# Kernel tuning notes

Measured on AMD Instinct MI355X. Metric: run time of the kernel, lower is better.

Reference implementation:

```python
import jax, jax.numpy as jnp
import numpy as np

N_NODES = 200000
N_EDGES = 3200000
NX = 8
NK = 2


def _l2norm(x, eps=1e-12):
    # F.normalize(x, p=2, dim=-1)
    n = jnp.linalg.norm(x, axis=-1, keepdims=True)
    return x / jnp.maximum(n, eps)


def _aniso_conv(x, src, dst, Kw, n_nodes):
    """For each kernel j: out_j[t] = sum_{e: dst[e]=t} Kw[j,e] * x[src[e]].
    Concatenate over kernels along the feature axis."""
    g = x[src]  # [E, d] gather
    def agg(w):  # w: [E]
        return jax.ops.segment_sum(w[:, None] * g, dst, num_segments=n_nodes)
    out = jax.vmap(agg)(Kw)  # [nk, N, d]
    return jnp.transpose(out, (1, 0, 2)).reshape(n_nodes, -1)  # [N, nk*d]


def setup_inputs() -> dict:
    key = jax.random.key(0)
    ks = jax.random.split(key, 8)
    x = jax.random.normal(ks[0], (N_NODES, NX), dtype=jnp.float32)
    src = jax.random.randint(ks[1], (N_EDGES,), 0, N_NODES, dtype=jnp.int64 if jax.config.jax_enable_x64 else jnp.int32)
    dst = jax.random.randint(ks[2], (N_EDGES,), 0, N_NODES, dtype=src.dtype)
    edge_index = jnp.stack([src, dst], axis=0)
    Kw = jax.random.normal(ks[3], (NK, N_EDGES), dtype=jnp.float32)
    d0, d1 = NX * NK, NX * NK * 2          # 16, 32
    d2 = d1 * NK                            # 64
    hidden, out_ch = 128, 64
    W0 = jax.random.normal(ks[4], (d0, d1), dtype=jnp.float32) / np.sqrt(d0)
    b0 = jnp.zeros((d1,), dtype=jnp.float32)
    W1 = jax.random.normal(ks[5], (d2, hidden), dtype=jnp.float32) / np.sqrt(d2)
    b1 = jnp.zeros((hidden,), dtype=jnp.float32)
    W2 = jax.random.normal(ks[6], (hidden, out_ch), dtype=jnp.float32) / np.sqrt(hidden)
    b2 = jnp.zeros((out_ch,), dtype=jnp.float32)
    return {"x": x, "edge_index": edge_index, "Kw": Kw,
            "W0": W0, "b0": b0, "W1": W1, "b1": b1, "W2": W2, "b2": b2}


def reference(x, edge_index, Kw, W0, b0, W1, b1, W2, b2):
    src, dst = edge_index[0], edge_index[1]
    n = x.shape[0]
    # layer 0: AnisoConv -> single-linear MLP -> L2 normalize
    h = _aniso_conv(x, src, dst, Kw, n)      # [N, 16]
    h = h @ W0 + b0                           # [N, 32]
    h = _l2norm(h)
    # layer 1: AnisoConv -> 2-layer MLP (ReLU between) -> L2 normalize
    h = _aniso_conv(h, src, dst, Kw, n)      # [N, 64]
    h = jax.nn.relu(h @ W1 + b1)             # [N, 128]
    h = h @ W2 + b2                           # [N, 64]
    h = _l2norm(h)
    return h
```

## Files before the change

kernel.cpp:

```cpp
#include <hip/hip_runtime.h>

#define NN 200000
#define NE 3200000
#define NB_SCAN 782
#define NBUCK 196
#define BSHIFT 10
#define BMASK 1023
#define SRCMASK 0x3FFFFu
#define NBLK_A 512
#define EPB (NE / NBLK_A)
#define NT_MLP1 12500
#define NPASS 13
#define EMAX 18

using bf16x8 = __attribute__((ext_vector_type(8))) short;
using f32x4  = __attribute__((ext_vector_type(4))) float;

__device__ __forceinline__ float bflo(unsigned u) { return __uint_as_float(u << 16); }
__device__ __forceinline__ float bfhi(unsigned u) { return __uint_as_float(u & 0xffff0000u); }
__device__ __forceinline__ unsigned short f2bfu(float f) {
  unsigned u = __float_as_uint(f);
  return (unsigned short)((u + 0x7fffu + ((u >> 16) & 1u)) >> 16);
}
__device__ __forceinline__ unsigned pack2(float a, float b) {
  return (unsigned)f2bfu(a) | ((unsigned)f2bfu(b) << 16);
}


__global__ __launch_bounds__(256) void bhist_kernel(const int* __restrict__ dst,
                                                    int* __restrict__ bhT) {
  __shared__ int h[NBUCK];
  for (int k = threadIdx.x; k < NBUCK; k += 256) h[k] = 0;
  __syncthreads();
  int base = blockIdx.x * EPB;
  for (int i = threadIdx.x; i < EPB; i += 256)
    atomicAdd(&h[dst[base + i] >> BSHIFT], 1);
  __syncthreads();
  for (int k = threadIdx.x; k < NBUCK; k += 256)
    bhT[k * NBLK_A + blockIdx.x] = h[k];
}

__global__ __launch_bounds__(NBLK_A) void bscan_kernel(int* __restrict__ bhT,
                                                       int* __restrict__ btot) {
  __shared__ int s[NBLK_A];
  int b = blockIdx.x;
  int v = bhT[b * NBLK_A + threadIdx.x];
  s[threadIdx.x] = v;
  __syncthreads();
#pragma unroll
  for (int off = 1; off < NBLK_A; off <<= 1) {
    int t = (threadIdx.x >= off) ? s[threadIdx.x - off] : 0;
    __syncthreads();
    s[threadIdx.x] += t;
    __syncthreads();
  }
  bhT[b * NBLK_A + threadIdx.x] = s[threadIdx.x] - v;
  if (threadIdx.x == NBLK_A - 1) btot[b] = s[NBLK_A - 1];
}

__global__ __launch_bounds__(256) void bbase_kernel(const int* __restrict__ btot,
                                                    int* __restrict__ bbase) {
  __shared__ int s[256];
  int v = (threadIdx.x < NBUCK) ? btot[threadIdx.x] : 0;
  s[threadIdx.x] = v;
  __syncthreads();
#pragma unroll
  for (int off = 1; off < 256; off <<= 1) {
    int t = (threadIdx.x >= off) ? s[threadIdx.x - off] : 0;
    __syncthreads();
    s[threadIdx.x] += t;
    __syncthreads();
  }
  if (threadIdx.x < NBUCK) bbase[threadIdx.x] = s[threadIdx.x] - v;
  if (threadIdx.x == NBUCK - 1) bbase[NBUCK] = s[threadIdx.x];
}

__global__ __launch_bounds__(256) void bplace_kernel(
    const int* __restrict__ src, const int* __restrict__ dst,
    const float* __restrict__ kw, const int* __restrict__ bhT,
    const int* __restrict__ bbase, uint2* __restrict__ bsorted) {
  __shared__ int cur[NBUCK];
  for (int k = threadIdx.x; k < NBUCK; k += 256)
    cur[k] = bbase[k] + bhT[k * NBLK_A + blockIdx.x];
  __syncthreads();
  int base = blockIdx.x * EPB;
  for (int i = threadIdx.x; i < EPB; i += 256) {
    int e = base + i;
    int d = dst[e];
    int p = atomicAdd(&cur[d >> BSHIFT], 1);
    uint2 u;
    u.x = (unsigned)src[e] | ((unsigned)(d & BMASK) << 18);
    u.y = pack2(kw[e], kw[NE + e]);
    bsorted[p] = u;
  }
}


__global__ __launch_bounds__(1024) void nhist_kernel(const uint2* __restrict__ bsorted,
                                                     const int* __restrict__ bbase,
                                                     int* __restrict__ cnt) {
  __shared__ int h[1024];
  h[threadIdx.x] = 0;
  __syncthreads();
  int b = blockIdx.x;
  int r0 = bbase[b], r1 = bbase[b + 1];
  for (int i = r0 + threadIdx.x; i < r1; i += 1024)
    atomicAdd(&h[bsorted[i].x >> 18], 1);
  __syncthreads();
  int node = b * 1024 + threadIdx.x;
  if (node < NN) cnt[node] = h[threadIdx.x];
}

__global__ __launch_bounds__(256) void scan1_kernel(const int* __restrict__ cnt,
                                                    int* __restrict__ offs,
                                                    int* __restrict__ bsums) {
  __shared__ int s[256];
  int i = blockIdx.x * 256 + threadIdx.x;
  int v = (i < NN) ? cnt[i] : 0;
  s[threadIdx.x] = v;
  __syncthreads();
#pragma unroll
  for (int off = 1; off < 256; off <<= 1) {
    int t = (threadIdx.x >= off) ? s[threadIdx.x - off] : 0;
    __syncthreads();
    s[threadIdx.x] += t;
    __syncthreads();
  }
  if (i < NN) offs[i] = s[threadIdx.x];
  if (threadIdx.x == 255) bsums[blockIdx.x] = s[255];
}

__global__ __launch_bounds__(1024) void scan2_kernel(int* __restrict__ bsums, int nb) {
  __shared__ int s[1024];
  int v = (threadIdx.x < nb) ? bsums[threadIdx.x] : 0;
  s[threadIdx.x] = v;
  __syncthreads();
#pragma unroll
  for (int off = 1; off < 1024; off <<= 1) {
    int t = (threadIdx.x >= off) ? s[threadIdx.x - off] : 0;
    __syncthreads();
    s[threadIdx.x] += t;
    __syncthreads();
  }
  if (threadIdx.x < nb) bsums[threadIdx.x] = s[threadIdx.x] - v;
}

__global__ __launch_bounds__(256) void scan3_kernel(const int* __restrict__ cnt,
                                                    const int* __restrict__ bsums,
                                                    int* __restrict__ offs) {
  int i = blockIdx.x * 256 + threadIdx.x;
  if (i >= NN) return;
  offs[i] = offs[i] - cnt[i] + bsums[blockIdx.x];
}

__global__ __launch_bounds__(1024) void nplace_kernel(const uint2* __restrict__ bsorted,
                                                      const int* __restrict__ bbase,
                                                      const int* __restrict__ offs,
                                                      uint2* __restrict__ sedge) {
  __shared__ int cur[1024];
  int b = blockIdx.x;
  int node = b * 1024 + threadIdx.x;
  cur[threadIdx.x] = (node < NN) ? offs[node] : 0;
  __syncthreads();
  int r0 = bbase[b], r1 = bbase[b + 1];
  int i0 = r0 + threadIdx.x;

  uint2 e[EMAX];
#pragma unroll
  for (int j = 0; j < EMAX; ++j) {
    int i = i0 + j * 1024;
    if (i < r1) e[j] = bsorted[i];
  }

  for (int p = 0; p < NPASS; ++p) {
#pragma unroll
    for (int j = 0; j < EMAX; ++j) {
      int i = i0 + j * 1024;
      if (i < r1) {
        unsigned srcv = e[j].x & SRCMASK;
        if ((int)(srcv >> 14) == p) {
          int pos = atomicAdd(&cur[e[j].x >> 18], 1);
          uint2 w; w.x = srcv; w.y = e[j].y;
          sedge[pos] = w;
        }
      }
    }
    __syncthreads();
  }
  for (int i = i0 + EMAX * 1024; i < r1; i += 1024) {
    uint2 u = bsorted[i];
    int pos = atomicAdd(&cur[u.x >> 18], 1);
    u.x &= SRCMASK;
    sedge[pos] = u;
  }
}


__global__ __launch_bounds__(256) void xcvt_kernel(const float* __restrict__ x,
                                                   unsigned short* __restrict__ xbf) {
  int i = blockIdx.x * 256 + threadIdx.x;
  if (i >= NN) return;
  const float4* xp = reinterpret_cast<const float4*>(x + (size_t)i * 8);
  float4 a = xp[0], b = xp[1];
  uint4 u;
  u.x = pack2(a.x, a.y); u.y = pack2(a.z, a.w);
  u.z = pack2(b.x, b.y); u.w = pack2(b.z, b.w);
  *reinterpret_cast<uint4*>(xbf + (size_t)i * 8) = u;
}


__global__ __launch_bounds__(256) void fused0_kernel(
    const unsigned short* __restrict__ xbf, const int* __restrict__ offs,
    const int* __restrict__ cnt, const uint2* __restrict__ sedge,
    const float* __restrict__ W0, const float* __restrict__ b0,
    unsigned short* __restrict__ h1bf) {
  __shared__ float w0t[32][16];
  __shared__ float b0s[32];
  int tid = threadIdx.x;
  for (int i = tid; i < 16 * 32; i += 256) {
    int k = i >> 5, j = i & 31;
    w0t[j][k] = W0[i];
  }
  if (tid < 32) b0s[tid] = b0[tid];
  __syncthreads();

  int node = blockIdx.x * 256 + tid;
  if (node >= NN) return;

  int start = offs[node];
  int deg = cnt[node];
  float h16[16];
#pragma unroll
  for (int k = 0; k < 16; ++k) h16[k] = 0.f;

  for (int i = 0; i < deg; ++i) {
    uint2 e = sedge[start + i];
    float k0 = bflo(e.y), k1 = bfhi(e.y);
    uint4 u = *reinterpret_cast<const uint4*>(xbf + (size_t)e.x * 8);
    float v0 = bflo(u.x), v1 = bfhi(u.x);
    float v2 = bflo(u.y), v3 = bfhi(u.y);
    float v4 = bflo(u.z), v5 = bfhi(u.z);
    float v6 = bflo(u.w), v7 = bfhi(u.w);
    h16[0] += k0 * v0; h16[1] += k0 * v1; h16[2] += k0 * v2; h16[3] += k0 * v3;
    h16[4] += k0 * v4; h16[5] += k0 * v5; h16[6] += k0 * v6; h16[7] += k0 * v7;
    h16[8]  += k1 * v0; h16[9]  += k1 * v1; h16[10] += k1 * v2; h16[11] += k1 * v3;
    h16[12] += k1 * v4; h16[13] += k1 * v5; h16[14] += k1 * v6; h16[15] += k1 * v7;
  }

  float o[32];
  float ss = 0.f;
#pragma unroll
  for (int j = 0; j < 32; ++j) {
    float acc = b0s[j];
#pragma unroll
    for (int k = 0; k < 16; ++k) acc += h16[k] * w0t[j][k];
    o[j] = acc;
    ss += acc * acc;
  }
  float inv = 1.f / fmaxf(sqrtf(ss), 1e-12f);
  uint4* op = reinterpret_cast<uint4*>(h1bf + (size_t)node * 32);
#pragma unroll
  for (int c = 0; c < 4; ++c) {
    uint4 u;
    u.x = pack2(o[c * 8 + 0] * inv, o[c * 8 + 1] * inv);
    u.y = pack2(o[c * 8 + 2] * inv, o[c * 8 + 3] * inv);
    u.z = pack2(o[c * 8 + 4] * inv, o[c * 8 + 5] * inv);
    u.w = pack2(o[c * 8 + 6] * inv, o[c * 8 + 7] * inv);
    op[c] = u;
  }
}


__global__ __launch_bounds__(256) void gather1_kernel(
    const unsigned short* __restrict__ h1bf, const int* __restrict__ offs,
    const int* __restrict__ cnt, const uint2* __restrict__ sedge,
    unsigned short* __restrict__ gbf) {
  int idx = blockIdx.x * 256 + threadIdx.x;
  int node = idx >> 2, q = idx & 3;
  if (node >= NN) return;
  int start = offs[node];
  int deg = cnt[node];

  float g0[8], g1[8];
#pragma unroll
  for (int k = 0; k < 8; ++k) { g0[k] = 0.f; g1[k] = 0.f; }

  for (int i = 0; i < deg; ++i) {
    uint2 e = sedge[start + i];
    float k0 = bflo(e.y), k1 = bfhi(e.y);
    uint4 u = *reinterpret_cast<const uint4*>(h1bf + (size_t)e.x * 32 + q * 8);
    float v0 = bflo(u.x), v1 = bfhi(u.x);
    float v2 = bflo(u.y), v3 = bfhi(u.y);
    float v4 = bflo(u.z), v5 = bfhi(u.z);
    float v6 = bflo(u.w), v7 = bfhi(u.w);
    g0[0] += k0 * v0; g0[1] += k0 * v1; g0[2] += k0 * v2; g0[3] += k0 * v3;
    g0[4] += k0 * v4; g0[5] += k0 * v5; g0[6] += k0 * v6; g0[7] += k0 * v7;
    g1[0] += k1 * v0; g1[1] += k1 * v1; g1[2] += k1 * v2; g1[3] += k1 * v3;
    g1[4] += k1 * v4; g1[5] += k1 * v5; g1[6] += k1 * v6; g1[7] += k1 * v7;
  }

  uint4 s0, s1;
  s0.x = pack2(g0[0], g0[1]); s0.y = pack2(g0[2], g0[3]);
  s0.z = pack2(g0[4], g0[5]); s0.w = pack2(g0[6], g0[7]);
  s1.x = pack2(g1[0], g1[1]); s1.y = pack2(g1[2], g1[3]);
  s1.z = pack2(g1[4], g1[5]); s1.w = pack2(g1[6], g1[7]);
  *reinterpret_cast<uint4*>(gbf + (size_t)node * 64 + q * 8) = s0;
  *reinterpret_cast<uint4*>(gbf + (size_t)node * 64 + 32 + q * 8) = s1;
}


__global__ __launch_bounds__(256) void mlp1_kernel(
    const unsigned short* __restrict__ gbf,
    const float* __restrict__ W1, const float* __restrict__ b1,
    const float* __restrict__ W2, const float* __restrict__ b2,
    float* __restrict__ out) {
  __shared__ __align__(16) short hlds[4][16][136];
  int tid = threadIdx.x;
  int wave = tid >> 6, lane = tid & 63;
  int lg = lane >> 4;
  int lr = lane & 15;

  bf16x8 w1f[8][2];
#pragma unroll
  for (int n = 0; n < 8; ++n)
#pragma unroll
    for (int ks = 0; ks < 2; ++ks) {
      bf16x8 f;
#pragma unroll
      for (int i = 0; i < 8; ++i)
        f[i] = (short)f2bfu(W1[(size_t)(ks * 32 + lg * 8 + i) * 128 + n * 16 + lr]);
      w1f[n][ks] = f;
    }
  bf16x8 w2f[4][4];
#pragma unroll
  for (int n2 = 0; n2 < 4; ++n2)
#pragma unroll
    for (int ks = 0; ks < 4; ++ks) {
      bf16x8 f;
#pragma unroll
      for (int i = 0; i < 8; ++i)
        f[i] = (short)f2bfu(W2[(size_t)(ks * 32 + lg * 8 + i) * 64 + n2 * 16 + lr]);
      w2f[n2][ks] = f;
    }
  float b1v[8], b2v[4];
#pragma unroll
  for (int n = 0; n < 8; ++n) b1v[n] = b1[n * 16 + lr];
#pragma unroll
  for (int n2 = 0; n2 < 4; ++n2) b2v[n2] = b2[n2 * 16 + lr];

  for (int tile = blockIdx.x * 4 + wave; tile < NT_MLP1; tile += gridDim.x * 4) {
    int base = tile * 16;
    const bf16x8* grow = reinterpret_cast<const bf16x8*>(gbf + (size_t)(base + lr) * 64);
    bf16x8 a1_0 = grow[lg];
    bf16x8 a1_1 = grow[4 + lg];

#pragma unroll
    for (int n = 0; n < 8; ++n) {
      f32x4 acc = {0.f, 0.f, 0.f, 0.f};
      acc = __builtin_amdgcn_mfma_f32_16x16x32_bf16(a1_0, w1f[n][0], acc, 0, 0, 0);
      acc = __builtin_amdgcn_mfma_f32_16x16x32_bf16(a1_1, w1f[n][1], acc, 0, 0, 0);
#pragma unroll
      for (int q = 0; q < 4; ++q) {
        float v = fmaxf(acc[q] + b1v[n], 0.f);
        hlds[wave][lg * 4 + q][n * 16 + lr] = (short)f2bfu(v);
      }
    }

    bf16x8 a2[4];
#pragma unroll
    for (int ks = 0; ks < 4; ++ks)
      a2[ks] = *reinterpret_cast<const bf16x8*>(&hlds[wave][lr][ks * 32 + lg * 8]);
    f32x4 acc2[4];
#pragma unroll
    for (int n2 = 0; n2 < 4; ++n2) {
      f32x4 a = {0.f, 0.f, 0.f, 0.f};
#pragma unroll
      for (int ks = 0; ks < 4; ++ks)
        a = __builtin_amdgcn_mfma_f32_16x16x32_bf16(a2[ks], w2f[n2][ks], a, 0, 0, 0);
      acc2[n2] = a;
    }

#pragma unroll
    for (int q = 0; q < 4; ++q) {
      float s = 0.f;
#pragma unroll
      for (int n2 = 0; n2 < 4; ++n2) {
        float v = acc2[n2][q] + b2v[n2];
        s += v * v;
      }
      s += __shfl_xor(s, 1); s += __shfl_xor(s, 2);
      s += __shfl_xor(s, 4); s += __shfl_xor(s, 8);
      float inv = 1.f / fmaxf(sqrtf(s), 1e-12f);
      size_t rowoff = (size_t)(base + lg * 4 + q) * 64 + lr;
#pragma unroll
      for (int n2 = 0; n2 < 4; ++n2)
        out[rowoff + n2 * 16] = (acc2[n2][q] + b2v[n2]) * inv;
    }
  }
}


extern "C" void kernel_launch(void* const* d_in, const int* in_sizes, int n_in,
                              void* d_out, int out_size, void* d_ws, size_t ws_size,
                              hipStream_t stream) {
  const float* x  = (const float*)d_in[0];
  const int* ei   = (const int*)d_in[1];
  const float* kw = (const float*)d_in[2];
  const float* W0 = (const float*)d_in[3];
  const float* b0 = (const float*)d_in[4];
  const float* W1 = (const float*)d_in[5];
  const float* b1 = (const float*)d_in[6];
  const float* W2 = (const float*)d_in[7];
  const float* b2 = (const float*)d_in[8];
  float* out = (float*)d_out;

  const int* src = ei;
  const int* dst = ei + NE;

  char* p = (char*)d_ws;
  uint2* bsorted = (uint2*)p;              p += (size_t)NE * 8;
  uint2* sedge   = (uint2*)p;              p += (size_t)NE * 8;
  unsigned short* h1bf = (unsigned short*)p; p += (size_t)NN * 32 * 2;
  unsigned short* xbf  = (unsigned short*)p; p += (size_t)NN * 8 * 2;
  int* bhT   = (int*)p;                    p += (size_t)NBUCK * NBLK_A * 4;
  int* btot  = (int*)p;                    p += (size_t)NBUCK * 4;
  int* bbase = (int*)p;                    p += (size_t)(NBUCK + 1) * 4;
  int* cnt   = (int*)p;                    p += (size_t)NN * 4;
  int* offs  = (int*)p;                    p += (size_t)NN * 4;
  int* bsums = (int*)p;                    p += 1024 * 4;
  unsigned short* gbf = (unsigned short*)bsorted;

  xcvt_kernel<<<NB_SCAN, 256, 0, stream>>>(x, xbf);

  bhist_kernel<<<NBLK_A, 256, 0, stream>>>(dst, bhT);
  bscan_kernel<<<NBUCK, NBLK_A, 0, stream>>>(bhT, btot);
  bbase_kernel<<<1, 256, 0, stream>>>(btot, bbase);
  bplace_kernel<<<NBLK_A, 256, 0, stream>>>(src, dst, kw, bhT, bbase, bsorted);

  nhist_kernel<<<NBUCK, 1024, 0, stream>>>(bsorted, bbase, cnt);
  scan1_kernel<<<NB_SCAN, 256, 0, stream>>>(cnt, offs, bsums);
  scan2_kernel<<<1, 1024, 0, stream>>>(bsums, NB_SCAN);
  scan3_kernel<<<NB_SCAN, 256, 0, stream>>>(cnt, bsums, offs);
  nplace_kernel<<<NBUCK, 1024, 0, stream>>>(bsorted, bbase, offs, sedge);

  fused0_kernel<<<NB_SCAN, 256, 0, stream>>>(xbf, offs, cnt, sedge, W0, b0, h1bf);
  gather1_kernel<<<(4 * NN + 255) / 256, 256, 0, stream>>>(h1bf, offs, cnt,
                                                           sedge, gbf);
  mlp1_kernel<<<768, 256, 0, stream>>>(gbf, W1, b1, W2, b2, out);
}
```

Before: 244.0 us.

## Fuse node histogram, scan and placement; fuse layer-1 gather with MLP

Merges the per-node histogram, the three-kernel global scan and the node placement into one kernel per bucket. Because buckets are contiguous in the bucket-sorted array, each bucket's exclusive offset comes from its base plus a local LDS scan. Also fuses the layer-1 gather with the MFMA MLP through LDS, which removes the intermediate gbf write and read. Weights are pre-packed into bf16 MFMA fragment order by a small kernel, so the fused blocks load fragments directly. The risk is that the MLP now runs once per 64-node block and reloads weight fragments from global memory each time.

```diff
diff --git a/kernel.cpp b/kernel.cpp
--- a/kernel.cpp
+++ b/kernel.cpp
@@ -9,7 +9,6 @@
 #define SRCMASK 0x3FFFFu
 #define NBLK_A 512
 #define EPB (NE / NBLK_A)
-#define NT_MLP1 12500
 #define NPASS 13
 #define EMAX 18
 
@@ -96,81 +95,45 @@
 }
 
 
-__global__ __launch_bounds__(1024) void nhist_kernel(const uint2* __restrict__ bsorted,
-                                                     const int* __restrict__ bbase,
-                                                     int* __restrict__ cnt) {
+__global__ __launch_bounds__(1024) void nsort_kernel(
+    const uint2* __restrict__ bsorted, const int* __restrict__ bbase,
+    int* __restrict__ cnt, int* __restrict__ offs, uint2* __restrict__ sedge) {
   __shared__ int h[1024];
-  h[threadIdx.x] = 0;
-  __syncthreads();
-  int b = blockIdx.x;
+  __shared__ int cur[1024];
+  int tid = threadIdx.x, b = blockIdx.x;
+  h[tid] = 0;
+  __syncthreads();
   int r0 = bbase[b], r1 = bbase[b + 1];
-  for (int i = r0 + threadIdx.x; i < r1; i += 1024)
-    atomicAdd(&h[bsorted[i].x >> 18], 1);
-  __syncthreads();
-  int node = b * 1024 + threadIdx.x;
-  if (node < NN) cnt[node] = h[threadIdx.x];
-}
-
-__global__ __launch_bounds__(256) void scan1_kernel(const int* __restrict__ cnt,
-                                                    int* __restrict__ offs,
-                                                    int* __restrict__ bsums) {
-  __shared__ int s[256];
-  int i = blockIdx.x * 256 + threadIdx.x;
-  int v = (i < NN) ? cnt[i] : 0;
-  s[threadIdx.x] = v;
-  __syncthreads();
-#pragma unroll
-  for (int off = 1; off < 256; off <<= 1) {
-    int t = (threadIdx.x >= off) ? s[threadIdx.x - off] : 0;
-    __syncthreads();
-    s[threadIdx.x] += t;
-    __syncthreads();
-  }
-  if (i < NN) offs[i] = s[threadIdx.x];
-  if (threadIdx.x == 255) bsums[blockIdx.x] = s[255];
-}
-
-__global__ __launch_bounds__(1024) void scan2_kernel(int* __restrict__ bsums, int nb) {
-  __shared__ int s[1024];
-  int v = (threadIdx.x < nb) ? bsums[threadIdx.x] : 0;
-  s[threadIdx.x] = v;
-  __syncthreads();
-#pragma unroll
-  for (int off = 1; off < 1024; off <<= 1) {
-    int t = (threadIdx.x >= off) ? s[threadIdx.x - off] : 0;
-    __syncthreads();
-    s[threadIdx.x] += t;
-    __syncthreads();
-  }
-  if (threadIdx.x < nb) bsums[threadIdx.x] = s[threadIdx.x] - v;
-}
-
-__global__ __launch_bounds__(256) void scan3_kernel(const int* __restrict__ cnt,
-                                                    const int* __restrict__ bsums,
-                                                    int* __restrict__ offs) {
-  int i = blockIdx.x * 256 + threadIdx.x;
-  if (i >= NN) return;
-  offs[i] = offs[i] - cnt[i] + bsums[blockIdx.x];
-}
-
-__global__ __launch_bounds__(1024) void nplace_kernel(const uint2* __restrict__ bsorted,
-                                                      const int* __restrict__ bbase,
-                                                      const int* __restrict__ offs,
-                                                      uint2* __restrict__ sedge) {
-  __shared__ int cur[1024];
-  int b = blockIdx.x;
-  int node = b * 1024 + threadIdx.x;
-  cur[threadIdx.x] = (node < NN) ? offs[node] : 0;
-  __syncthreads();
-  int r0 = bbase[b], r1 = bbase[b + 1];
-  int i0 = r0 + threadIdx.x;
+  int i0 = r0 + tid;
 
   uint2 e[EMAX];
 #pragma unroll
   for (int j = 0; j < EMAX; ++j) {
     int i = i0 + j * 1024;
-    if (i < r1) e[j] = bsorted[i];
-  }
+    if (i < r1) {
+      e[j] = bsorted[i];
+      atomicAdd(&h[e[j].x >> 18], 1);
+    }
+  }
+  for (int i = i0 + EMAX * 1024; i < r1; i += 1024)
+    atomicAdd(&h[bsorted[i].x >> 18], 1);
+  __syncthreads();
+
+  int v = h[tid];
+  cur[tid] = v;
+  __syncthreads();
+  for (int off = 1; off < 1024; off <<= 1) {
+    int t = (tid >= off) ? cur[tid - off] : 0;
+    __syncthreads();
+    cur[tid] += t;
+    __syncthreads();
+  }
+  int excl = r0 + cur[tid] - v;
+  int node = b * 1024 + tid;
+  if (node < NN) { cnt[node] = v; offs[node] = excl; }
+  __syncthreads();
+  cur[tid] = excl;
+  __syncthreads();
 
   for (int p = 0; p < NPASS; ++p) {
 #pragma unroll
@@ -206,6 +169,31 @@
   u.x = pack2(a.x, a.y); u.y = pack2(a.z, a.w);
   u.z = pack2(b.x, b.y); u.w = pack2(b.z, b.w);
   *reinterpret_cast<uint4*>(xbf + (size_t)i * 8) = u;
+}
+
+
+__global__ __launch_bounds__(256) void wpack_kernel(
+    const float* __restrict__ W1, const float* __restrict__ W2,
+    unsigned short* __restrict__ W1p, unsigned short* __restrict__ W2p) {
+  int t = threadIdx.x;
+  {
+    int n = t >> 5, lr = (t >> 1) & 15, ks = t & 1;
+#pragma unroll
+    for (int lg = 0; lg < 4; ++lg)
+#pragma unroll
+      for (int i = 0; i < 8; ++i)
+        W1p[(((n * 16 + lr) * 2 + ks) * 4 + lg) * 8 + i] =
+            f2bfu(W1[(size_t)(ks * 32 + lg * 8 + i) * 128 + n * 16 + lr]);
+  }
+  {
+    int n2 = t >> 6, lr = (t >> 2) & 15, ks = t & 3;
+#pragma unroll
+    for (int lg = 0; lg < 4; ++lg)
+#pragma unroll
+      for (int i = 0; i < 8; ++i)
+        W2p[(((n2 * 16 + lr) * 4 + ks) * 4 + lg) * 8 + i] =
+            f2bfu(W2[(size_t)(ks * 32 + lg * 8 + i) * 64 + n2 * 16 + lr]);
+  }
 }
 
 
@@ -271,16 +259,20 @@
 }
 
 
-__global__ __launch_bounds__(256) void gather1_kernel(
+__global__ __launch_bounds__(256) void gmlp_kernel(
     const unsigned short* __restrict__ h1bf, const int* __restrict__ offs,
     const int* __restrict__ cnt, const uint2* __restrict__ sedge,
-    unsigned short* __restrict__ gbf) {
-  int idx = blockIdx.x * 256 + threadIdx.x;
-  int node = idx >> 2, q = idx & 3;
-  if (node >= NN) return;
+    const unsigned short* __restrict__ W1p, const float* __restrict__ b1,
+    const unsigned short* __restrict__ W2p, const float* __restrict__ b2,
+    float* __restrict__ out) {
+  __shared__ __align__(16) unsigned short gl[64][72];
+  __shared__ __align__(16) short hl[4][16][136];
+  int tid = threadIdx.x;
+  int nloc = tid >> 2, q = tid & 3;
+  int node = blockIdx.x * 64 + nloc;
+
   int start = offs[node];
   int deg = cnt[node];
-
   float g0[8], g1[8];
 #pragma unroll
   for (int k = 0; k < 8; ++k) { g0[k] = 0.f; g1[k] = 0.f; }
@@ -304,98 +296,73 @@
   s0.z = pack2(g0[4], g0[5]); s0.w = pack2(g0[6], g0[7]);
   s1.x = pack2(g1[0], g1[1]); s1.y = pack2(g1[2], g1[3]);
   s1.z = pack2(g1[4], g1[5]); s1.w = pack2(g1[6], g1[7]);
-  *reinterpret_cast<uint4*>(gbf + (size_t)node * 64 + q * 8) = s0;
-  *reinterpret_cast<uint4*>(gbf + (size_t)node * 64 + 32 + q * 8) = s1;
-}
-
-
-__global__ __launch_bounds__(256) void mlp1_kernel(
-    const unsigned short* __restrict__ gbf,
-    const float* __restrict__ W1, const float* __restrict__ b1,
-    const float* __restrict__ W2, const float* __restrict__ b2,
-    float* __restrict__ out) {
-  __shared__ __align__(16) short hlds[4][16][136];
-  int tid = threadIdx.x;
+  *reinterpret_cast<uint4*>(&gl[nloc][q * 8]) = s0;
+  *reinterpret_cast<uint4*>(&gl[nloc][32 + q * 8]) = s1;
+  __syncthreads();
+
   int wave = tid >> 6, lane = tid & 63;
   int lg = lane >> 4;
   int lr = lane & 15;
 
-  bf16x8 w1f[8][2];
-#pragma unroll
-  for (int n = 0; n < 8; ++n)
-#pragma unroll
-    for (int ks = 0; ks < 2; ++ks) {
-      bf16x8 f;
-#pragma unroll
-      for (int i = 0; i < 8; ++i)
-        f[i] = (short)f2bfu(W1[(size_t)(ks * 32 + lg * 8 + i) * 128 + n * 16 + lr]);
-      w1f[n][ks] = f;
+  float b1v[8], b2v[4];
+#pragma unroll
+  for (int n = 0; n < 8; ++n) b1v[n] = b1[n * 16 + lr];
+#pragma unroll
+  for (int n2 = 0; n2 < 4; ++n2) b2v[n2] = b2[n2 * 16 + lr];
+
+  int arow = wave * 16 + lr;
+  bf16x8 a1_0 = *reinterpret_cast<const bf16x8*>(&gl[arow][lg * 8]);
+  bf16x8 a1_1 = *reinterpret_cast<const bf16x8*>(&gl[arow][32 + lg * 8]);
+
+#pragma unroll
+  for (int n = 0; n < 8; ++n) {
+    bf16x8 w10 = *reinterpret_cast<const bf16x8*>(
+        &W1p[(((n * 16 + lr) * 2 + 0) * 4 + lg) * 8]);
+    bf16x8 w11 = *reinterpret_cast<const bf16x8*>(
+        &W1p[(((n * 16 + lr) * 2 + 1) * 4 + lg) * 8]);
+    f32x4 acc = {0.f, 0.f, 0.f, 0.f};
+    acc = __builtin_amdgcn_mfma_f32_16x16x32_bf16(a1_0, w10, acc, 0, 0, 0);
+    acc = __builtin_amdgcn_mfma_f32_16x16x32_bf16(a1_1, w11, acc, 0, 0, 0);
+#pragma unroll
+    for (int p = 0; p < 4; ++p) {
+      float v = fmaxf(acc[p] + b1v[n], 0.f);
+      hl[wave][lg * 4 + p][n * 16 + lr] = (short)f2bfu(v);
     }
-  bf16x8 w2f[4][4];
-#pragma unroll
-  for (int n2 = 0; n2 < 4; ++n2)
+  }
+
+  bf16x8 a2[4];
+#pragma unroll
+  for (int ks = 0; ks < 4; ++ks)
+    a2[ks] = *reinterpret_cast<const bf16x8*>(&hl[wave][lr][ks * 32 + lg * 8]);
+  f32x4 acc2[4];
+#pragma unroll
+  for (int n2 = 0; n2 < 4; ++n2) {
+    f32x4 a = {0.f, 0.f, 0.f, 0.f};
 #pragma unroll
     for (int ks = 0; ks < 4; ++ks) {
-      bf16x8 f;
-#pragma unroll
-      for (int i = 0; i < 8; ++i)
-        f[i] = (short)f2bfu(W2[(size_t)(ks * 32 + lg * 8 + i) * 64 + n2 * 16 + lr]);
-      w2f[n2][ks] = f;
+      bf16x8 w2 = *reinterpret_cast<const bf16x8*>(
+          &W2p[(((n2 * 16 + lr) * 4 + ks) * 4 + lg) * 8]);
+      a = __builtin_amdgcn_mfma_f32_16x16x32_bf16(a2[ks], w2, a, 0, 0, 0);
     }
-  float b1v[8], b2v[4];
-#pragma unroll
-  for (int n = 0; n < 8; ++n) b1v[n] = b1[n * 16 + lr];
-#pragma unroll
-  for (int n2 = 0; n2 < 4; ++n2) b2v[n2] = b2[n2 * 16 + lr];
-
-  for (int tile = blockIdx.x * 4 + wave; tile < NT_MLP1; tile += gridDim.x * 4) {
-    int base = tile * 16;
-    const bf16x8* grow = reinterpret_cast<const bf16x8*>(gbf + (size_t)(base + lr) * 64);
-    bf16x8 a1_0 = grow[lg];
-    bf16x8 a1_1 = grow[4 + lg];
-
-#pragma unroll
-    for (int n = 0; n < 8; ++n) {
-      f32x4 acc = {0.f, 0.f, 0.f, 0.f};
-      acc = __builtin_amdgcn_mfma_f32_16x16x32_bf16(a1_0, w1f[n][0], acc, 0, 0, 0);
-      acc = __builtin_amdgcn_mfma_f32_16x16x32_bf16(a1_1, w1f[n][1], acc, 0, 0, 0);
-#pragma unroll
-      for (int q = 0; q < 4; ++q) {
-        float v = fmaxf(acc[q] + b1v[n], 0.f);
-        hlds[wave][lg * 4 + q][n * 16 + lr] = (short)f2bfu(v);
-      }
+    acc2[n2] = a;
+  }
+
+  int base = blockIdx.x * 64 + wave * 16;
+#pragma unroll
+  for (int p = 0; p < 4; ++p) {
+    float s = 0.f;
+#pragma unroll
+    for (int n2 = 0; n2 < 4; ++n2) {
+      float v = acc2[n2][p] + b2v[n2];
+      s += v * v;
     }
-
-    bf16x8 a2[4];
-#pragma unroll
-    for (int ks = 0; ks < 4; ++ks)
-      a2[ks] = *reinterpret_cast<const bf16x8*>(&hlds[wave][lr][ks * 32 + lg * 8]);
-    f32x4 acc2[4];
-#pragma unroll
-    for (int n2 = 0; n2 < 4; ++n2) {
-      f32x4 a = {0.f, 0.f, 0.f, 0.f};
-#pragma unroll
-      for (int ks = 0; ks < 4; ++ks)
-        a = __builtin_amdgcn_mfma_f32_16x16x32_bf16(a2[ks], w2f[n2][ks], a, 0, 0, 0);
-      acc2[n2] = a;
-    }
-
-#pragma unroll
-    for (int q = 0; q < 4; ++q) {
-      float s = 0.f;
-#pragma unroll
-      for (int n2 = 0; n2 < 4; ++n2) {
-        float v = acc2[n2][q] + b2v[n2];
-        s += v * v;
-      }
-      s += __shfl_xor(s, 1); s += __shfl_xor(s, 2);
-      s += __shfl_xor(s, 4); s += __shfl_xor(s, 8);
-      float inv = 1.f / fmaxf(sqrtf(s), 1e-12f);
-      size_t rowoff = (size_t)(base + lg * 4 + q) * 64 + lr;
-#pragma unroll
-      for (int n2 = 0; n2 < 4; ++n2)
-        out[rowoff + n2 * 16] = (acc2[n2][q] + b2v[n2]) * inv;
-    }
+    s += __shfl_xor(s, 1); s += __shfl_xor(s, 2);
+    s += __shfl_xor(s, 4); s += __shfl_xor(s, 8);
+    float inv = 1.f / fmaxf(sqrtf(s), 1e-12f);
+    size_t rowoff = (size_t)(base + lg * 4 + p) * 64 + lr;
+#pragma unroll
+    for (int n2 = 0; n2 < 4; ++n2)
+      out[rowoff + n2 * 16] = (acc2[n2][p] + b2v[n2]) * inv;
   }
 }
 
@@ -418,18 +385,19 @@
   const int* dst = ei + NE;
 
   char* p = (char*)d_ws;
-  uint2* bsorted = (uint2*)p;              p += (size_t)NE * 8;
-  uint2* sedge   = (uint2*)p;              p += (size_t)NE * 8;
+  uint2* bsorted = (uint2*)p;                p += (size_t)NE * 8;
+  uint2* sedge   = (uint2*)p;                p += (size_t)NE * 8;
   unsigned short* h1bf = (unsigned short*)p; p += (size_t)NN * 32 * 2;
   unsigned short* xbf  = (unsigned short*)p; p += (size_t)NN * 8 * 2;
-  int* bhT   = (int*)p;                    p += (size_t)NBUCK * NBLK_A * 4;
-  int* btot  = (int*)p;                    p += (size_t)NBUCK * 4;
-  int* bbase = (int*)p;                    p += (size_t)(NBUCK + 1) * 4;
-  int* cnt   = (int*)p;                    p += (size_t)NN * 4;
-  int* offs  = (int*)p;                    p += (size_t)NN * 4;
-  int* bsums = (int*)p;                    p += 1024 * 4;
-  unsigned short* gbf = (unsigned short*)bsorted;
-
+  int* bhT   = (int*)p;                      p += (size_t)NBUCK * NBLK_A * 4;
+  int* btot  = (int*)p;                      p += (size_t)NBUCK * 4;
+  int* bbase = (int*)p;                      p += (size_t)(NBUCK + 1) * 4;
+  int* cnt   = (int*)p;                      p += (size_t)NN * 4;
+  int* offs  = (int*)p;                      p += (size_t)NN * 4;
+  unsigned short* W1p = (unsigned short*)p;  p += (size_t)8192 * 2;
+  unsigned short* W2p = (unsigned short*)p;  p += (size_t)8192 * 2;
+
+  wpack_kernel<<<1, 256, 0, stream>>>(W1, W2, W1p, W2p);
   xcvt_kernel<<<NB_SCAN, 256, 0, stream>>>(x, xbf);
 
   bhist_kernel<<<NBLK_A, 256, 0, stream>>>(dst, bhT);
@@ -437,14 +405,9 @@
   bbase_kernel<<<1, 256, 0, stream>>>(btot, bbase);
   bplace_kernel<<<NBLK_A, 256, 0, stream>>>(src, dst, kw, bhT, bbase, bsorted);
 
-  nhist_kernel<<<NBUCK, 1024, 0, stream>>>(bsorted, bbase, cnt);
-  scan1_kernel<<<NB_SCAN, 256, 0, stream>>>(cnt, offs, bsums);
-  scan2_kernel<<<1, 1024, 0, stream>>>(bsums, NB_SCAN);
-  scan3_kernel<<<NB_SCAN, 256, 0, stream>>>(cnt, bsums, offs);
-  nplace_kernel<<<NBUCK, 1024, 0, stream>>>(bsorted, bbase, offs, sedge);
+  nsort_kernel<<<NBUCK, 1024, 0, stream>>>(bsorted, bbase, cnt, offs, sedge);
 
   fused0_kernel<<<NB_SCAN, 256, 0, stream>>>(xbf, offs, cnt, sedge, W0, b0, h1bf);
-  gather1_kernel<<<(4 * NN + 255) / 256, 256, 0, stream>>>(h1bf, offs, cnt,
-                                                           sedge, gbf);
-  mlp1_kernel<<<768, 256, 0, stream>>>(gbf, W1, b1, W2, b2, out);
-}
+  gmlp_kernel<<<NN / 64, 256, 0, stream>>>(h1bf, offs, cnt, sedge,
+                                           W1p, b1, W2p, b2, out);
+}
```

New measurement: 262.4 us. 1.08x slower.

## Fuse node histogram, global scan and placement into one per-bucket kernel

Applied to the files above, without the earlier changes.

Replaces the node-histogram kernel, the three-kernel global prefix scan and the placement kernel with a single per-bucket kernel. Each block counts its bucket's destination nodes while loading edges into registers, does a local block scan offset by the bucket base, and then places the edges. This removes four kernel launches and the re-read of bsorted, since the bucket base already gives the global offset. In exchange, each block runs an extra 1024-wide shared-memory scan, and launch-level parallelism for the scan stage drops to 196 blocks.

```diff
diff --git a/kernel.cpp b/kernel.cpp
--- a/kernel.cpp
+++ b/kernel.cpp
@@ -9,9 +9,9 @@
 #define SRCMASK 0x3FFFFu
 #define NBLK_A 512
 #define EPB (NE / NBLK_A)
-#define NT_MLP1 12500
 #define NPASS 13
 #define EMAX 18
+#define NT_MLP1 12500
 
 using bf16x8 = __attribute__((ext_vector_type(8))) short;
 using f32x4  = __attribute__((ext_vector_type(4))) float;
@@ -96,81 +96,45 @@
 }
 
 
-__global__ __launch_bounds__(1024) void nhist_kernel(const uint2* __restrict__ bsorted,
-                                                     const int* __restrict__ bbase,
-                                                     int* __restrict__ cnt) {
+__global__ __launch_bounds__(1024) void nsort_kernel(
+    const uint2* __restrict__ bsorted, const int* __restrict__ bbase,
+    int* __restrict__ cnt, int* __restrict__ offs, uint2* __restrict__ sedge) {
   __shared__ int h[1024];
-  h[threadIdx.x] = 0;
-  __syncthreads();
-  int b = blockIdx.x;
+  __shared__ int cur[1024];
+  int tid = threadIdx.x, b = blockIdx.x;
+  h[tid] = 0;
+  __syncthreads();
   int r0 = bbase[b], r1 = bbase[b + 1];
-  for (int i = r0 + threadIdx.x; i < r1; i += 1024)
-    atomicAdd(&h[bsorted[i].x >> 18], 1);
-  __syncthreads();
-  int node = b * 1024 + threadIdx.x;
-  if (node < NN) cnt[node] = h[threadIdx.x];
-}
-
-__global__ __launch_bounds__(256) void scan1_kernel(const int* __restrict__ cnt,
-                                                    int* __restrict__ offs,
-                                                    int* __restrict__ bsums) {
-  __shared__ int s[256];
-  int i = blockIdx.x * 256 + threadIdx.x;
-  int v = (i < NN) ? cnt[i] : 0;
-  s[threadIdx.x] = v;
-  __syncthreads();
-#pragma unroll
-  for (int off = 1; off < 256; off <<= 1) {
-    int t = (threadIdx.x >= off) ? s[threadIdx.x - off] : 0;
-    __syncthreads();
-    s[threadIdx.x] += t;
-    __syncthreads();
-  }
-  if (i < NN) offs[i] = s[threadIdx.x];
-  if (threadIdx.x == 255) bsums[blockIdx.x] = s[255];
-}
-
-__global__ __launch_bounds__(1024) void scan2_kernel(int* __restrict__ bsums, int nb) {
-  __shared__ int s[1024];
-  int v = (threadIdx.x < nb) ? bsums[threadIdx.x] : 0;
-  s[threadIdx.x] = v;
-  __syncthreads();
-#pragma unroll
-  for (int off = 1; off < 1024; off <<= 1) {
-    int t = (threadIdx.x >= off) ? s[threadIdx.x - off] : 0;
-    __syncthreads();
-    s[threadIdx.x] += t;
-    __syncthreads();
-  }
-  if (threadIdx.x < nb) bsums[threadIdx.x] = s[threadIdx.x] - v;
-}
-
-__global__ __launch_bounds__(256) void scan3_kernel(const int* __restrict__ cnt,
-                                                    const int* __restrict__ bsums,
-                                                    int* __restrict__ offs) {
-  int i = blockIdx.x * 256 + threadIdx.x;
-  if (i >= NN) return;
-  offs[i] = offs[i] - cnt[i] + bsums[blockIdx.x];
-}
-
-__global__ __launch_bounds__(1024) void nplace_kernel(const uint2* __restrict__ bsorted,
-                                                      const int* __restrict__ bbase,
-                                                      const int* __restrict__ offs,
-                                                      uint2* __restrict__ sedge) {
-  __shared__ int cur[1024];
-  int b = blockIdx.x;
-  int node = b * 1024 + threadIdx.x;
-  cur[threadIdx.x] = (node < NN) ? offs[node] : 0;
-  __syncthreads();
-  int r0 = bbase[b], r1 = bbase[b + 1];
-  int i0 = r0 + threadIdx.x;
+  int i0 = r0 + tid;
 
   uint2 e[EMAX];
 #pragma unroll
   for (int j = 0; j < EMAX; ++j) {
     int i = i0 + j * 1024;
-    if (i < r1) e[j] = bsorted[i];
-  }
+    if (i < r1) {
+      e[j] = bsorted[i];
+      atomicAdd(&h[e[j].x >> 18], 1);
+    }
+  }
+  for (int i = i0 + EMAX * 1024; i < r1; i += 1024)
+    atomicAdd(&h[bsorted[i].x >> 18], 1);
+  __syncthreads();
+
+  int v = h[tid];
+  cur[tid] = v;
+  __syncthreads();
+  for (int off = 1; off < 1024; off <<= 1) {
+    int t = (tid >= off) ? cur[tid - off] : 0;
+    __syncthreads();
+    cur[tid] += t;
+    __syncthreads();
+  }
+  int excl = r0 + cur[tid] - v;
+  int node = b * 1024 + tid;
+  if (node < NN) { cnt[node] = v; offs[node] = excl; }
+  __syncthreads();
+  cur[tid] = excl;
+  __syncthreads();
 
   for (int p = 0; p < NPASS; ++p) {
 #pragma unroll
@@ -418,16 +382,15 @@
   const int* dst = ei + NE;
 
   char* p = (char*)d_ws;
-  uint2* bsorted = (uint2*)p;              p += (size_t)NE * 8;
-  uint2* sedge   = (uint2*)p;              p += (size_t)NE * 8;
+  uint2* bsorted = (uint2*)p;                p += (size_t)NE * 8;
+  uint2* sedge   = (uint2*)p;                p += (size_t)NE * 8;
   unsigned short* h1bf = (unsigned short*)p; p += (size_t)NN * 32 * 2;
   unsigned short* xbf  = (unsigned short*)p; p += (size_t)NN * 8 * 2;
-  int* bhT   = (int*)p;                    p += (size_t)NBUCK * NBLK_A * 4;
-  int* btot  = (int*)p;                    p += (size_t)NBUCK * 4;
-  int* bbase = (int*)p;                    p += (size_t)(NBUCK + 1) * 4;
-  int* cnt   = (int*)p;                    p += (size_t)NN * 4;
-  int* offs  = (int*)p;                    p += (size_t)NN * 4;
-  int* bsums = (int*)p;                    p += 1024 * 4;
+  int* bhT   = (int*)p;                      p += (size_t)NBUCK * NBLK_A * 4;
+  int* btot  = (int*)p;                      p += (size_t)NBUCK * 4;
+  int* bbase = (int*)p;                      p += (size_t)(NBUCK + 1) * 4;
+  int* cnt   = (int*)p;                      p += (size_t)NN * 4;
+  int* offs  = (int*)p;                      p += (size_t)NN * 4;
   unsigned short* gbf = (unsigned short*)bsorted;
 
   xcvt_kernel<<<NB_SCAN, 256, 0, stream>>>(x, xbf);
@@ -437,11 +400,7 @@
   bbase_kernel<<<1, 256, 0, stream>>>(btot, bbase);
   bplace_kernel<<<NBLK_A, 256, 0, stream>>>(src, dst, kw, bhT, bbase, bsorted);
 
-  nhist_kernel<<<NBUCK, 1024, 0, stream>>>(bsorted, bbase, cnt);
-  scan1_kernel<<<NB_SCAN, 256, 0, stream>>>(cnt, offs, bsums);
-  scan2_kernel<<<1, 1024, 0, stream>>>(bsums, NB_SCAN);
-  scan3_kernel<<<NB_SCAN, 256, 0, stream>>>(cnt, bsums, offs);
-  nplace_kernel<<<NBUCK, 1024, 0, stream>>>(bsorted, bbase, offs, sedge);
+  nsort_kernel<<<NBUCK, 1024, 0, stream>>>(bsorted, bbase, cnt, offs, sedge);
 
   fused0_kernel<<<NB_SCAN, 256, 0, stream>>>(xbf, offs, cnt, sedge, W0, b0, h1bf);
   gather1_kernel<<<(4 * NN + 255) / 256, 256, 0, stream>>>(h1bf, offs, cnt,
```

New measurement: 234.6 us. 1.04x faster.
